# Performance work log

Hardware: AMD Instinct MI355X
Metric: run time of the kernel (lower is better)

The kernel has to match this reference:

```python
import jax, jax.numpy as jnp
import numpy as np

K = 24            # kNN neighbors per DynamicEdgeConv (includes self, dist 0)
N_PER_GRAPH = 128 # uniform nodes per graph
N_GRAPHS = 128
N_IN = 16
HID = 128
N_OUT = 6


def _knn_idx(xg, k):
    # xg: [G, N, D] -> indices of k nearest neighbors per node, [G, N, k]
    sq = jnp.sum(xg * xg, axis=-1)                       # [G, N]
    d2 = sq[:, :, None] + sq[:, None, :] - 2.0 * jnp.einsum('gnd,gmd->gnm', xg, xg)
    _, idx = jax.lax.top_k(-d2, k)                       # smallest distances
    return idx


def _dynamic_edge_conv(xg, w, b, k=K):
    # DynamicEdgeConv: recompute kNN on current features, edge MLP on
    # [x_i, x_j - x_i], max-aggregate over neighbors.
    idx = _knn_idx(xg, k)                                # [G, N, k]
    x_j = jax.vmap(lambda v, i: v[i])(xg, idx)           # [G, N, k, D]
    x_i = xg[:, :, None, :]                              # [G, N, 1, D]
    e = jnp.concatenate([jnp.broadcast_to(x_i, x_j.shape), x_j - x_i], axis=-1)
    h = jax.nn.elu(jnp.einsum('gnkf,fh->gnkh', e, w) + b)
    return jnp.max(h, axis=2)                            # [G, N, H]


def _linear(x, w, b):
    return x @ w + b


def setup_inputs() -> dict:
    key = jax.random.key(0)
    ks = jax.random.split(key, 16)

    def W(k, fi, fo):
        return (jax.random.normal(k, (fi, fo), dtype=jnp.float32) / np.sqrt(fi)).astype(jnp.float32)

    inp = {
        'x_pf': jax.random.normal(ks[0], (N_GRAPHS * N_PER_GRAPH, N_IN), dtype=jnp.float32),
        'enc_w1': W(ks[1], N_IN, HID),  'enc_b1': jnp.zeros((HID,), jnp.float32),
        'enc_w2': W(ks[2], HID, HID),   'enc_b2': jnp.zeros((HID,), jnp.float32),
        'conv1_w': W(ks[3], 2 * HID, HID), 'conv1_b': jnp.zeros((HID,), jnp.float32),
        'conv2_w': W(ks[4], 2 * HID, HID), 'conv2_b': jnp.zeros((HID,), jnp.float32),
        'conv3_w': W(ks[5], 2 * HID, HID), 'conv3_b': jnp.zeros((HID,), jnp.float32),
        'out_w1': W(ks[6], HID, 64), 'out_b1': jnp.zeros((64,), jnp.float32),
        'out_w2': W(ks[7], 64, 32),  'out_b2': jnp.zeros((32,), jnp.float32),
        'out_w3': W(ks[8], 32, 32),  'out_b3': jnp.zeros((32,), jnp.float32),
        'out_w4': W(ks[9], 32, N_OUT), 'out_b4': jnp.zeros((N_OUT,), jnp.float32),
        'batch_pf': jnp.repeat(jnp.arange(N_GRAPHS, dtype=jnp.int64 if jax.config.jax_enable_x64 else jnp.int32), N_PER_GRAPH),
    }
    return inp


def reference(x_pf, enc_w1, enc_b1, enc_w2, enc_b2,
              conv1_w, conv1_b, conv2_w, conv2_b, conv3_w, conv3_b,
              out_w1, out_b1, out_w2, out_b2, out_w3, out_b3, out_w4, out_b4,
              batch_pf):
    G = x_pf.shape[0] // N_PER_GRAPH
    # pf_encode: Linear -> ELU -> Linear -> ELU
    h = jax.nn.elu(_linear(x_pf, enc_w1, enc_b1))
    h = jax.nn.elu(_linear(h, enc_w2, enc_b2))
    hg = h.reshape(G, N_PER_GRAPH, HID)  # uniform graphs; batch_pf = repeat(arange(G))
    hg = _dynamic_edge_conv(hg, conv1_w, conv1_b)
    hg = _dynamic_edge_conv(hg, conv2_w, conv2_b)
    hg = _dynamic_edge_conv(hg, conv3_w, conv3_b)
    # global_add_pool over nodes of each graph
    pooled = jnp.sum(hg, axis=1)                          # [G, HID]
    o = jax.nn.elu(_linear(pooled, out_w1, out_b1))
    o = jax.nn.elu(_linear(o, out_w2, out_b2))
    o = jax.nn.elu(_linear(o, out_w3, out_b3))
    o = _linear(o, out_w4, out_b4)
    return (o, batch_pf)
```

## Files before the change

kernel.cpp:

```cpp
#include <hip/hip_runtime.h>
#include <hip/hip_fp16.h>
#include <hip/hip_bf16.h>
#include <cmath>

#define G_NUM 128
#define NPTS  128
#define FDIM  128
#define KNNK  24
#define NTOT  (G_NUM*NPTS)

typedef short s8v __attribute__((ext_vector_type(8)));
typedef float f32x4 __attribute__((ext_vector_type(4)));

__device__ __forceinline__ float eluf(float x){ return x > 0.0f ? x : expm1f(x); }

__device__ __forceinline__ unsigned short f2bf(float f) {
    unsigned int u = __float_as_uint(f);
    unsigned int r = (u + 0x7fffu + ((u >> 16) & 1u)) >> 16;
    return (unsigned short)r;
}
__device__ __forceinline__ float bf2f(unsigned short b) {
    return __uint_as_float(((unsigned int)b) << 16);
}

__global__ void prep_kernel(const float* __restrict__ w1, const float* __restrict__ w2,
                            const float* __restrict__ w3, const float* __restrict__ ew2,
                            const float* __restrict__ b1, const float* __restrict__ b2,
                            const float* __restrict__ b3,
                            unsigned short* __restrict__ wcatT,
                            unsigned short* __restrict__ enc2T,
                            float* __restrict__ bias,
                            const int* __restrict__ bpf,
                            float* __restrict__ out)
{
    int e = blockIdx.x * 256 + threadIdx.x;
    if (e < 16384) out[768 + e] = (float)bpf[e];
    if (e < 98304) {
        int l = e >> 15;
        int r = e & 32767;
        int k = r >> 8;
        int n = r & 255;
        const float* w = (l == 0) ? w1 : ((l == 1) ? w2 : w3);
        float v = (n < 128) ? (w[k * 128 + n] - w[(128 + k) * 128 + n])
                            : w[(128 + k) * 128 + (n - 128)];
        wcatT[l * 32768 + n * 128 + k] = f2bf(v);
    } else if (e < 114688) {
        int i = e - 98304;
        int k = i >> 7, n = i & 127;
        enc2T[n * 128 + k] = f2bf(ew2[k * 128 + n]);
    } else if (e < 115456) {
        int j = e - 114688;
        int l = j >> 8, c = j & 255;
        const float* b = (l == 0) ? b1 : ((l == 1) ? b2 : b3);
        bias[l * 256 + c] = (c < 128) ? b[c] : 0.0f;
    }
}

template<int DOELU>
__global__ __launch_bounds__(256) void gemmT(const float* __restrict__ A,
                                             const unsigned short* __restrict__ Bt,
                                             const float* __restrict__ bias,
                                             float* __restrict__ C0,
                                             float* __restrict__ C1)
{
    extern __shared__ char smc[];
    const int tid = threadIdx.x;
    const int m0 = blockIdx.x * 128;
    const unsigned short* Btg = Bt + (size_t)blockIdx.y * 16384;
    const float* bg = bias + blockIdx.y * 128;
    float* C = blockIdx.y ? C1 : C0;

    for (int e = tid; e < 4096; e += 256) {
        int m = e >> 5, q = e & 31;
        float4 v = *reinterpret_cast<const float4*>(&A[(size_t)(m0 + m) * 128 + 4 * q]);
        ushort4 p;
        p.x = f2bf(v.x); p.y = f2bf(v.y); p.z = f2bf(v.z); p.w = f2bf(v.w);
        int byte = (m * 256 + q * 8) ^ ((m & 15) << 4);
        *reinterpret_cast<ushort4*>(smc + byte) = p;
    }
    for (int e = tid; e < 2048; e += 256) {
        int n = e >> 4, q = e & 15;
        uint4 v = *reinterpret_cast<const uint4*>(Btg + n * 128 + q * 8);
        int byte = (n * 256 + q * 16) ^ ((n & 15) << 4);
        *reinterpret_cast<uint4*>(smc + 32768 + byte) = v;
    }
    __syncthreads();

    const int l = tid & 63, w = tid >> 6;
    const int wr = w >> 1, wc = w & 1;
    const int lr = l & 15, lg = l >> 4;

    f32x4 acc[4][4] = {};
    #pragma unroll
    for (int ks = 0; ks < 4; ++ks) {
        s8v a_f[4], b_f[4];
        #pragma unroll
        for (int mi = 0; mi < 4; ++mi) {
            int row = wr * 64 + mi * 16 + lr;
            int byte = (row * 256 + ks * 64 + lg * 16) ^ ((row & 15) << 4);
            a_f[mi] = *reinterpret_cast<const s8v*>(smc + byte);
        }
        #pragma unroll
        for (int ni = 0; ni < 4; ++ni) {
            int n = wc * 64 + ni * 16 + lr;
            int byte = (n * 256 + ks * 64 + lg * 16) ^ ((n & 15) << 4);
            b_f[ni] = *reinterpret_cast<const s8v*>(smc + 32768 + byte);
        }
        #pragma unroll
        for (int mi = 0; mi < 4; ++mi)
            #pragma unroll
            for (int ni = 0; ni < 4; ++ni)
                acc[mi][ni] = __builtin_amdgcn_mfma_f32_16x16x32_bf16(
                    a_f[mi], b_f[ni], acc[mi][ni], 0, 0, 0);
    }

    float bl[4];
    #pragma unroll
    for (int ni = 0; ni < 4; ++ni) bl[ni] = bg[wc * 64 + ni * 16 + lr];

    #pragma unroll
    for (int mi = 0; mi < 4; ++mi) {
        int rbase = m0 + wr * 64 + mi * 16 + lg * 4;
        #pragma unroll
        for (int ni = 0; ni < 4; ++ni) {
            int col = wc * 64 + ni * 16 + lr;
            #pragma unroll
            for (int q = 0; q < 4; ++q) {
                float v = acc[mi][ni][q] + bl[ni];
                if (DOELU) v = eluf(v);
                C[(size_t)(rbase + q) * 128 + col] = v;
            }
        }
    }
}

template<int KD, int TM, int DOELU>
__global__ __launch_bounds__(256) void gemm2(const float* __restrict__ A, int lda,
                                             const float* __restrict__ B, int ldb,
                                             const float* __restrict__ bias,
                                             float* __restrict__ C0)
{
    extern __shared__ float sm[];
    float* As = sm;
    float* Bs = sm + TM * (KD + 1);
    const int tid = threadIdx.x;
    const int m0 = blockIdx.x * TM;
    float* C = C0;
    const float* bg = bias;

    constexpr int NF4 = KD / 4;
    for (int e = tid; e < TM * NF4; e += 256) {
        int q = e % NF4, m = e / NF4;
        float4 v = *reinterpret_cast<const float4*>(&A[(size_t)(m0 + m) * lda + 4 * q]);
        float* dst = &As[m * (KD + 1) + 4 * q];
        dst[0] = v.x; dst[1] = v.y; dst[2] = v.z; dst[3] = v.w;
    }
    for (int e = tid; e < KD * 32; e += 256) {
        int q = e & 31, k = e >> 5;
        float4 v = *reinterpret_cast<const float4*>(&B[(size_t)k * ldb + 4 * q]);
        float* dst = &Bs[k * 129 + 4 * q];
        dst[0] = v.x; dst[1] = v.y; dst[2] = v.z; dst[3] = v.w;
    }
    __syncthreads();

    const int tml = tid & 15;
    const int tnh = tid >> 4;
    constexpr int NR = TM / 16;
    float acc[NR][8] = {};
    #pragma unroll 4
    for (int k = 0; k < KD; ++k) {
        float av[NR], bv[8];
        #pragma unroll
        for (int s = 0; s < NR; ++s) av[s] = As[(tml + 16 * s) * (KD + 1) + k];
        #pragma unroll
        for (int u = 0; u < 8; ++u) bv[u] = Bs[k * 129 + tnh + 16 * u];
        #pragma unroll
        for (int s = 0; s < NR; ++s)
            #pragma unroll
            for (int u = 0; u < 8; ++u) acc[s][u] += av[s] * bv[u];
    }
    __syncthreads();
    float* Ce = sm;
    #pragma unroll
    for (int s = 0; s < NR; ++s)
        #pragma unroll
        for (int u = 0; u < 8; ++u)
            Ce[(tml + 16 * s) * 132 + tnh + 16 * u] = acc[s][u];
    __syncthreads();
    for (int e = tid; e < TM * 32; e += 256) {
        int q = e & 31, m = e >> 5;
        float4 v = *reinterpret_cast<const float4*>(&Ce[m * 132 + 4 * q]);
        float4 b4 = *reinterpret_cast<const float4*>(&bg[4 * q]);
        v.x += b4.x; v.y += b4.y; v.z += b4.z; v.w += b4.w;
        if (DOELU) { v.x = eluf(v.x); v.y = eluf(v.y); v.z = eluf(v.z); v.w = eluf(v.w); }
        *reinterpret_cast<float4*>(&C[(size_t)(m0 + m) * 128 + 4 * q]) = v;
    }
}

#define XHI_OFF 0
#define XLO_OFF 32768
#define D_OFF   65536
#define SQ_OFF  99328
#define IDX_OFF 99840
#define CC_OFF  105984
#define EDGE_LDS 138752

__global__ __launch_bounds__(512) void edge_kernel(const float* __restrict__ hin,
                                                   const float* __restrict__ cc,
                                                   float* __restrict__ hio)
{
    extern __shared__ char smc[];
    float* D  = (float*)(smc + D_OFF);
    float* Sq = (float*)(smc + SQ_OFF);
    unsigned int* idxL = (unsigned int*)(smc + IDX_OFF);
    unsigned int* Cc   = (unsigned int*)(smc + CC_OFF);

    const int g = blockIdx.x >> 1, half = blockIdx.x & 1;
    const int r0 = half * 64;
    const int tid = threadIdx.x;
    const float* hg = hin + (size_t)g * NPTS * FDIM;
    const float* cg = cc  + (size_t)g * NPTS * FDIM;
    float* og = hio + (size_t)g * NPTS * FDIM;

    {
        const int m = tid >> 2;
        const int k0 = (tid & 3) * 32;
        float sq = 0.f;
        #pragma unroll
        for (int i = 0; i < 8; ++i) {
            float4 v = *reinterpret_cast<const float4*>(&hg[m * 128 + k0 + 4 * i]);
            ushort4 hi, lo;
            hi.x = f2bf(v.x); lo.x = f2bf(v.x - bf2f(hi.x));
            hi.y = f2bf(v.y); lo.y = f2bf(v.y - bf2f(hi.y));
            hi.z = f2bf(v.z); lo.z = f2bf(v.z - bf2f(hi.z));
            hi.w = f2bf(v.w); lo.w = f2bf(v.w - bf2f(hi.w));
            sq += v.x * v.x + v.y * v.y + v.z * v.z + v.w * v.w;
            int byte = (m * 256 + (k0 + 4 * i) * 2) ^ ((m & 15) << 4);
            *reinterpret_cast<ushort4*>(smc + XHI_OFF + byte) = hi;
            *reinterpret_cast<ushort4*>(smc + XLO_OFF + byte) = lo;
        }
        sq += __shfl_xor(sq, 1);
        sq += __shfl_xor(sq, 2);
        if ((tid & 3) == 0) Sq[m] = sq;
    }
    __syncthreads();

    if (tid < 256) {
        const int w = tid >> 6;
        const int l = tid & 63;
        const int lr = l & 15, lg = l >> 4;
        const int arow = r0 + w * 16 + lr;
        const int aswz = (arow & 15) << 4;

        f32x4 acc[8] = {};
        #pragma unroll
        for (int ks = 0; ks < 4; ++ks) {
            int abyte = (arow * 256 + ks * 64 + lg * 16) ^ aswz;
            s8v ahi = *reinterpret_cast<const s8v*>(smc + XHI_OFF + abyte);
            s8v alo = *reinterpret_cast<const s8v*>(smc + XLO_OFF + abyte);
            #pragma unroll
            for (int ni = 0; ni < 8; ++ni) {
                int brow = ni * 16 + lr;
                int bbyte = (brow * 256 + ks * 64 + lg * 16) ^ ((brow & 15) << 4);
                s8v bhi = *reinterpret_cast<const s8v*>(smc + XHI_OFF + bbyte);
                s8v blo = *reinterpret_cast<const s8v*>(smc + XLO_OFF + bbyte);
                acc[ni] = __builtin_amdgcn_mfma_f32_16x16x32_bf16(alo, bhi, acc[ni], 0, 0, 0);
                acc[ni] = __builtin_amdgcn_mfma_f32_16x16x32_bf16(ahi, blo, acc[ni], 0, 0, 0);
                acc[ni] = __builtin_amdgcn_mfma_f32_16x16x32_bf16(ahi, bhi, acc[ni], 0, 0, 0);
            }
        }
        float sqa[4];
        #pragma unroll
        for (int q = 0; q < 4; ++q) sqa[q] = Sq[r0 + w * 16 + lg * 4 + q];
        #pragma unroll
        for (int ni = 0; ni < 8; ++ni) {
            float sqc = Sq[ni * 16 + lr];
            #pragma unroll
            for (int q = 0; q < 4; ++q)
                D[(w * 16 + lg * 4 + q) * 132 + ni * 16 + lr] =
                    sqa[q] + sqc - 2.f * acc[ni][q];
        }
    } else {
        for (int e = tid - 256; e < 4096; e += 256) {
            int q = e & 31, j = e >> 5;
            float4 v = *reinterpret_cast<const float4*>(&cg[j * 128 + 4 * q]);
            unsigned int p0 = ((unsigned int)__half_as_ushort(__float2half(v.y)) << 16)
                            |  (unsigned int)__half_as_ushort(__float2half(v.x));
            unsigned int p1 = ((unsigned int)__half_as_ushort(__float2half(v.w)) << 16)
                            |  (unsigned int)__half_as_ushort(__float2half(v.z));
            Cc[j * 64 + 2 * q]     = p0;
            Cc[j * 64 + 2 * q + 1] = p1;
        }
    }
    __syncthreads();

    const int w8 = tid >> 6, l = tid & 63;

    for (int lr2 = w8 * 8; lr2 < w8 * 8 + 8; ++lr2) {
        float2 cur = *reinterpret_cast<const float2*>(&D[lr2 * 132 + 2 * l]);
        unsigned int ub0 = __float_as_uint(cur.x);
        unsigned int ub1 = __float_as_uint(cur.y);
        unsigned int u0 = (ub0 & 0x80000000u) ? ~ub0 : (ub0 | 0x80000000u);
        unsigned int u1 = (ub1 & 0x80000000u) ? ~ub1 : (ub1 | 0x80000000u);

        bool c0 = true, c1 = true, in0 = false, in1 = false;
        int need = KNNK;
        for (int b = 31; b >= 0; --b) {
            bool z0 = c0 && !((u0 >> b) & 1u);
            bool z1 = c1 && !((u1 >> b) & 1u);
            int cnt = __popcll(__ballot(z0)) + __popcll(__ballot(z1));
            if (cnt > need) { c0 = z0; c1 = z1; }
            else if (cnt == need) { in0 |= z0; in1 |= z1; need = 0; break; }
            else { in0 |= z0; in1 |= z1; need -= cnt;
                   c0 = c0 && !z0; c1 = c1 && !z1; }
        }
        if (need > 0) {
            unsigned long long m0 = __ballot(c0), m1 = __ballot(c1);
            unsigned long long below = (1ull << l) - 1ull;
            int rk0 = __popcll(m0 & below) + __popcll(m1 & below);
            int rk1 = rk0 + (int)((m0 >> l) & 1ull);
            in0 = in0 || (c0 && rk0 < need);
            in1 = in1 || (c1 && rk1 < need);
        }
        unsigned long long f0 = __ballot(in0), f1 = __ballot(in1);
        int cnt0 = __popcll(f0);
        unsigned long long below = (1ull << l) - 1ull;
        if (in0) idxL[lr2 * KNNK + __popcll(f0 & below)] = 2 * l;
        if (in1) idxL[lr2 * KNNK + cnt0 + __popcll(f1 & below)] = 2 * l + 1;
    }

    {
        const int hh = l >> 5, j = l & 31;
        #pragma unroll
        for (int u = 0; u < 4; ++u) {
            const int r = w8 * 8 + 2 * u + hh;
            const unsigned int* il = &idxL[r * KNNK];
            float mc0 = -3.0e38f, mc1 = -3.0e38f, mc2 = -3.0e38f, mc3 = -3.0e38f;
            #pragma unroll
            for (int t = 0; t < KNNK; t += 4) {
                unsigned int p0 = il[t], p1 = il[t + 1], p2 = il[t + 2], p3 = il[t + 3];
                uint2 a = *reinterpret_cast<const uint2*>(&Cc[p0 * 64 + 2 * j]);
                uint2 b = *reinterpret_cast<const uint2*>(&Cc[p1 * 64 + 2 * j]);
                uint2 c = *reinterpret_cast<const uint2*>(&Cc[p2 * 64 + 2 * j]);
                uint2 d = *reinterpret_cast<const uint2*>(&Cc[p3 * 64 + 2 * j]);
                mc0 = fmaxf(fmaxf(mc0,
                        __half2float(__ushort_as_half((unsigned short)(a.x & 0xffffu)))),
                        fmaxf(__half2float(__ushort_as_half((unsigned short)(b.x & 0xffffu))),
                              fmaxf(__half2float(__ushort_as_half((unsigned short)(c.x & 0xffffu))),
                                    __half2float(__ushort_as_half((unsigned short)(d.x & 0xffffu))))));
                mc1 = fmaxf(fmaxf(mc1,
                        __half2float(__ushort_as_half((unsigned short)(a.x >> 16)))),
                        fmaxf(__half2float(__ushort_as_half((unsigned short)(b.x >> 16))),
                              fmaxf(__half2float(__ushort_as_half((unsigned short)(c.x >> 16))),
                                    __half2float(__ushort_as_half((unsigned short)(d.x >> 16))))));
                mc2 = fmaxf(fmaxf(mc2,
                        __half2float(__ushort_as_half((unsigned short)(a.y & 0xffffu)))),
                        fmaxf(__half2float(__ushort_as_half((unsigned short)(b.y & 0xffffu))),
                              fmaxf(__half2float(__ushort_as_half((unsigned short)(c.y & 0xffffu))),
                                    __half2float(__ushort_as_half((unsigned short)(d.y & 0xffffu))))));
                mc3 = fmaxf(fmaxf(mc3,
                        __half2float(__ushort_as_half((unsigned short)(a.y >> 16)))),
                        fmaxf(__half2float(__ushort_as_half((unsigned short)(b.y >> 16))),
                              fmaxf(__half2float(__ushort_as_half((unsigned short)(c.y >> 16))),
                                    __half2float(__ushort_as_half((unsigned short)(d.y >> 16))))));
            }
            float4 av = *reinterpret_cast<const float4*>(&og[(r0 + r) * 128 + 4 * j]);
            float4 o;
            o.x = eluf(av.x + mc0);
            o.y = eluf(av.y + mc1);
            o.z = eluf(av.z + mc2);
            o.w = eluf(av.w + mc3);
            *reinterpret_cast<float4*>(&og[(r0 + r) * 128 + 4 * j]) = o;
        }
    }
}

__global__ __launch_bounds__(512) void head_kernel(const float* __restrict__ h,
        const float* __restrict__ w1, const float* __restrict__ b1,
        const float* __restrict__ w2, const float* __restrict__ b2,
        const float* __restrict__ w3, const float* __restrict__ b3,
        const float* __restrict__ w4, const float* __restrict__ b4,
        float* __restrict__ out)
{
    __shared__ float ps[4][128];
    __shared__ float pooled[128], s1[64], s2[32], s3[32];
    const int g = blockIdx.x, t = threadIdx.x;
    const float* hg = h + (size_t)g * NPTS * FDIM;
    const int f = t & 127, hp = t >> 7;
    float s = 0.0f;
    for (int p = 0; p < 32; ++p) s += hg[(hp * 32 + p) * 128 + f];
    ps[hp][f] = s;
    __syncthreads();
    if (t < 128) pooled[t] = ps[0][t] + ps[1][t] + ps[2][t] + ps[3][t];
    __syncthreads();
    if (t < 64) {
        float a = b1[t];
        #pragma unroll 8
        for (int k = 0; k < 128; ++k) a += pooled[k] * w1[k * 64 + t];
        s1[t] = eluf(a);
    }
    __syncthreads();
    if (t < 32) {
        float a = b2[t];
        #pragma unroll 8
        for (int k = 0; k < 64; ++k) a += s1[k] * w2[k * 32 + t];
        s2[t] = eluf(a);
    }
    __syncthreads();
    if (t < 32) {
        float a = b3[t];
        #pragma unroll 8
        for (int k = 0; k < 32; ++k) a += s2[k] * w3[k * 32 + t];
        s3[t] = eluf(a);
    }
    __syncthreads();
    if (t < 6) {
        float a = b4[t];
        #pragma unroll 8
        for (int k = 0; k < 32; ++k) a += s3[k] * w4[k * 6 + t];
        out[g * 6 + t] = a;
    }
}

extern "C" void kernel_launch(void* const* d_in, const int* in_sizes, int n_in,
                              void* d_out, int out_size, void* d_ws, size_t ws_size,
                              hipStream_t stream)
{
    const float* x_pf   = (const float*)d_in[0];
    const float* enc_w1 = (const float*)d_in[1];
    const float* enc_b1 = (const float*)d_in[2];
    const float* enc_w2 = (const float*)d_in[3];
    const float* enc_b2 = (const float*)d_in[4];
    const float* c1w = (const float*)d_in[5];
    const float* c1b = (const float*)d_in[6];
    const float* c2w = (const float*)d_in[7];
    const float* c2b = (const float*)d_in[8];
    const float* c3w = (const float*)d_in[9];
    const float* c3b = (const float*)d_in[10];
    const float* o_w1 = (const float*)d_in[11];
    const float* o_b1 = (const float*)d_in[12];
    const float* o_w2 = (const float*)d_in[13];
    const float* o_b2 = (const float*)d_in[14];
    const float* o_w3 = (const float*)d_in[15];
    const float* o_b3 = (const float*)d_in[16];
    const float* o_w4 = (const float*)d_in[17];
    const float* o_b4 = (const float*)d_in[18];
    const int*   bpf  = (const int*)d_in[19];
    float* out = (float*)d_out;

    float* ws   = (float*)d_ws;
    float* h_a  = ws;
    float* h_b  = h_a + (size_t)NTOT * FDIM;
    float* ac_c = h_b + (size_t)NTOT * FDIM;
    unsigned short* wcatT = (unsigned short*)(ac_c + (size_t)NTOT * FDIM);
    unsigned short* enc2T = wcatT + 3 * 32768;
    float* biasF = (float*)(enc2T + 16384);

    prep_kernel<<<451, 256, 0, stream>>>(c1w, c2w, c3w, enc_w2,
                                         c1b, c2b, c3b, wcatT, enc2T, biasF,
                                         bpf, out);

    gemm2<16, 64, 1><<<dim3(NTOT / 64, 1), 256, 8448 * 4, stream>>>(
        x_pf, 16, enc_w1, 128, enc_b1, ac_c);
    gemmT<1><<<dim3(NTOT / 128, 1), 256, 65536, stream>>>(
        ac_c, enc2T, enc_b2, h_a, nullptr);

    float* hc = h_a;
    float* hn = h_b;
    for (int l = 0; l < 3; ++l) {
        gemmT<0><<<dim3(NTOT / 128, 2), 256, 65536, stream>>>(
            hc, wcatT + (size_t)l * 32768, biasF + l * 256, hn, ac_c);
        edge_kernel<<<2 * G_NUM, 512, EDGE_LDS, stream>>>(hc, ac_c, hn);
        float* t = hc; hc = hn; hn = t;
    }

    head_kernel<<<G_NUM, 512, 0, stream>>>(hc, o_w1, o_b1, o_w2, o_b2, o_w3, o_b3,
                                           o_w4, o_b4, out);
}
```

Baseline: 298.8 us.

## Fuse per-layer edge-conv GEMMs into the kNN/aggregation kernel

Removes the separate gemmT launch that computed x_i-part and x_j-part projections to global memory. The edge kernel now computes both projections in-block with MFMA from the bf16 node features already in LDS, reading weights straight from global. The neighbor projections go to fp16 in LDS and the self term to fp32 in LDS. This cuts global round-trips and one launch per layer, at the cost of redundant neighbor-projection work across the two half-graph blocks and uncached weight loads. LDS row padding is also changed to reduce bank conflicts.

```diff
diff --git a/kernel.cpp b/kernel.cpp
--- a/kernel.cpp
+++ b/kernel.cpp
@@ -60,15 +60,12 @@
 __global__ __launch_bounds__(256) void gemmT(const float* __restrict__ A,
                                              const unsigned short* __restrict__ Bt,
                                              const float* __restrict__ bias,
-                                             float* __restrict__ C0,
-                                             float* __restrict__ C1)
+                                             float* __restrict__ C0)
 {
     extern __shared__ char smc[];
     const int tid = threadIdx.x;
     const int m0 = blockIdx.x * 128;
-    const unsigned short* Btg = Bt + (size_t)blockIdx.y * 16384;
-    const float* bg = bias + blockIdx.y * 128;
-    float* C = blockIdx.y ? C1 : C0;
+    float* C = C0;
 
     for (int e = tid; e < 4096; e += 256) {
         int m = e >> 5, q = e & 31;
@@ -80,7 +77,7 @@
     }
     for (int e = tid; e < 2048; e += 256) {
         int n = e >> 4, q = e & 15;
-        uint4 v = *reinterpret_cast<const uint4*>(Btg + n * 128 + q * 8);
+        uint4 v = *reinterpret_cast<const uint4*>(Bt + n * 128 + q * 8);
         int byte = (n * 256 + q * 16) ^ ((n & 15) << 4);
         *reinterpret_cast<uint4*>(smc + 32768 + byte) = v;
     }
@@ -116,7 +113,7 @@
 
     float bl[4];
     #pragma unroll
-    for (int ni = 0; ni < 4; ++ni) bl[ni] = bg[wc * 64 + ni * 16 + lr];
+    for (int ni = 0; ni < 4; ++ni) bl[ni] = bias[wc * 64 + ni * 16 + lr];
 
     #pragma unroll
     for (int mi = 0; mi < 4; ++mi) {
@@ -200,27 +197,28 @@
 #define XHI_OFF 0
 #define XLO_OFF 32768
 #define D_OFF   65536
-#define SQ_OFF  99328
-#define IDX_OFF 99840
-#define CC_OFF  105984
-#define EDGE_LDS 138752
-
-__global__ __launch_bounds__(512) void edge_kernel(const float* __restrict__ hin,
-                                                   const float* __restrict__ cc,
-                                                   float* __restrict__ hio)
+#define CC_OFF  98816
+#define IDX_OFF 132608
+#define SQ_OFF  138752
+#define CONV_LDS 139264
+
+__global__ __launch_bounds__(512) void conv_fused(const float* __restrict__ hin,
+                                                  const unsigned short* __restrict__ wT,
+                                                  const float* __restrict__ bias,
+                                                  float* __restrict__ hout)
 {
     extern __shared__ char smc[];
     float* D  = (float*)(smc + D_OFF);
     float* Sq = (float*)(smc + SQ_OFF);
     unsigned int* idxL = (unsigned int*)(smc + IDX_OFF);
     unsigned int* Cc   = (unsigned int*)(smc + CC_OFF);
+    float* Al = (float*)(smc + XLO_OFF);
 
     const int g = blockIdx.x >> 1, half = blockIdx.x & 1;
     const int r0 = half * 64;
     const int tid = threadIdx.x;
     const float* hg = hin + (size_t)g * NPTS * FDIM;
-    const float* cg = cc  + (size_t)g * NPTS * FDIM;
-    float* og = hio + (size_t)g * NPTS * FDIM;
+    float* og = hout + (size_t)g * NPTS * FDIM;
 
     {
         const int m = tid >> 2;
@@ -245,13 +243,12 @@
     }
     __syncthreads();
 
-    if (tid < 256) {
-        const int w = tid >> 6;
-        const int l = tid & 63;
-        const int lr = l & 15, lg = l >> 4;
+    const int l = tid & 63, w = tid >> 6;
+    const int lr = l & 15, lg = l >> 4;
+
+    if (w < 4) {
         const int arow = r0 + w * 16 + lr;
         const int aswz = (arow & 15) << 4;
-
         f32x4 acc[8] = {};
         #pragma unroll
         for (int ks = 0; ks < 4; ++ks) {
@@ -277,27 +274,79 @@
             float sqc = Sq[ni * 16 + lr];
             #pragma unroll
             for (int q = 0; q < 4; ++q)
-                D[(w * 16 + lg * 4 + q) * 132 + ni * 16 + lr] =
+                D[(w * 16 + lg * 4 + q) * 130 + ni * 16 + lr] =
                     sqa[q] + sqc - 2.f * acc[ni][q];
         }
     } else {
-        for (int e = tid - 256; e < 4096; e += 256) {
-            int q = e & 31, j = e >> 5;
-            float4 v = *reinterpret_cast<const float4*>(&cg[j * 128 + 4 * q]);
-            unsigned int p0 = ((unsigned int)__half_as_ushort(__float2half(v.y)) << 16)
-                            |  (unsigned int)__half_as_ushort(__float2half(v.x));
-            unsigned int p1 = ((unsigned int)__half_as_ushort(__float2half(v.w)) << 16)
-                            |  (unsigned int)__half_as_ushort(__float2half(v.z));
-            Cc[j * 64 + 2 * q]     = p0;
-            Cc[j * 64 + 2 * q + 1] = p1;
-        }
-    }
-    __syncthreads();
-
-    const int w8 = tid >> 6, l = tid & 63;
-
-    for (int lr2 = w8 * 8; lr2 < w8 * 8 + 8; ++lr2) {
-        float2 cur = *reinterpret_cast<const float2*>(&D[lr2 * 132 + 2 * l]);
+        const int w4 = w - 4;
+        f32x4 acc[2][8] = {};
+        #pragma unroll
+        for (int ks = 0; ks < 4; ++ks) {
+            s8v a_f[2];
+            #pragma unroll
+            for (int m2 = 0; m2 < 2; ++m2) {
+                int row = (2 * w4 + m2) * 16 + lr;
+                int byte = (row * 256 + ks * 64 + lg * 16) ^ ((row & 15) << 4);
+                a_f[m2] = *reinterpret_cast<const s8v*>(smc + XHI_OFF + byte);
+            }
+            #pragma unroll
+            for (int ni = 0; ni < 8; ++ni) {
+                int n = 128 + ni * 16 + lr;
+                s8v b = *reinterpret_cast<const s8v*>(wT + n * 128 + ks * 32 + lg * 8);
+                #pragma unroll
+                for (int m2 = 0; m2 < 2; ++m2)
+                    acc[m2][ni] = __builtin_amdgcn_mfma_f32_16x16x32_bf16(
+                        a_f[m2], b, acc[m2][ni], 0, 0, 0);
+            }
+        }
+        #pragma unroll
+        for (int m2 = 0; m2 < 2; ++m2)
+            #pragma unroll
+            for (int ni = 0; ni < 8; ++ni)
+                #pragma unroll
+                for (int q = 0; q < 4; ++q) {
+                    float v = acc[m2][ni][q];
+                    float p = __shfl_xor(v, 1);
+                    if (!(lr & 1)) {
+                        unsigned int u =
+                            ((unsigned int)__half_as_ushort(__float2half(p)) << 16)
+                          |  (unsigned int)__half_as_ushort(__float2half(v));
+                        int j = (2 * w4 + m2) * 16 + lg * 4 + q;
+                        Cc[j * 66 + ni * 8 + (lr >> 1)] = u;
+                    }
+                }
+    }
+    __syncthreads();
+
+    {
+        const int mt = w >> 1;
+        const int nb = (w & 1) * 4;
+        f32x4 acc[4] = {};
+        const int arow = r0 + mt * 16 + lr;
+        const int aswz = (arow & 15) << 4;
+        #pragma unroll
+        for (int ks = 0; ks < 4; ++ks) {
+            int abyte = (arow * 256 + ks * 64 + lg * 16) ^ aswz;
+            s8v a_f = *reinterpret_cast<const s8v*>(smc + XHI_OFF + abyte);
+            #pragma unroll
+            for (int ni = 0; ni < 4; ++ni) {
+                int n = (nb + ni) * 16 + lr;
+                s8v b = *reinterpret_cast<const s8v*>(wT + n * 128 + ks * 32 + lg * 8);
+                acc[ni] = __builtin_amdgcn_mfma_f32_16x16x32_bf16(a_f, b, acc[ni], 0, 0, 0);
+            }
+        }
+        #pragma unroll
+        for (int ni = 0; ni < 4; ++ni) {
+            int h = (nb + ni) * 16 + lr;
+            float bl = bias[h];
+            #pragma unroll
+            for (int q = 0; q < 4; ++q)
+                Al[(mt * 16 + lg * 4 + q) * 128 + h] = acc[ni][q] + bl;
+        }
+    }
+
+    for (int lr2 = w * 8; lr2 < w * 8 + 8; ++lr2) {
+        float2 cur = *reinterpret_cast<const float2*>(&D[lr2 * 130 + 2 * l]);
         unsigned int ub0 = __float_as_uint(cur.x);
         unsigned int ub1 = __float_as_uint(cur.y);
         unsigned int u0 = (ub0 & 0x80000000u) ? ~ub0 : (ub0 | 0x80000000u);
@@ -328,21 +377,22 @@
         if (in0) idxL[lr2 * KNNK + __popcll(f0 & below)] = 2 * l;
         if (in1) idxL[lr2 * KNNK + cnt0 + __popcll(f1 & below)] = 2 * l + 1;
     }
+    __syncthreads();
 
     {
-        const int hh = l >> 5, j = l & 31;
+        const int hh = l >> 5, jl = l & 31;
         #pragma unroll
         for (int u = 0; u < 4; ++u) {
-            const int r = w8 * 8 + 2 * u + hh;
+            const int r = w * 8 + 2 * u + hh;
             const unsigned int* il = &idxL[r * KNNK];
             float mc0 = -3.0e38f, mc1 = -3.0e38f, mc2 = -3.0e38f, mc3 = -3.0e38f;
             #pragma unroll
             for (int t = 0; t < KNNK; t += 4) {
                 unsigned int p0 = il[t], p1 = il[t + 1], p2 = il[t + 2], p3 = il[t + 3];
-                uint2 a = *reinterpret_cast<const uint2*>(&Cc[p0 * 64 + 2 * j]);
-                uint2 b = *reinterpret_cast<const uint2*>(&Cc[p1 * 64 + 2 * j]);
-                uint2 c = *reinterpret_cast<const uint2*>(&Cc[p2 * 64 + 2 * j]);
-                uint2 d = *reinterpret_cast<const uint2*>(&Cc[p3 * 64 + 2 * j]);
+                uint2 a = *reinterpret_cast<const uint2*>(&Cc[p0 * 66 + 2 * jl]);
+                uint2 b = *reinterpret_cast<const uint2*>(&Cc[p1 * 66 + 2 * jl]);
+                uint2 c = *reinterpret_cast<const uint2*>(&Cc[p2 * 66 + 2 * jl]);
+                uint2 d = *reinterpret_cast<const uint2*>(&Cc[p3 * 66 + 2 * jl]);
                 mc0 = fmaxf(fmaxf(mc0,
                         __half2float(__ushort_as_half((unsigned short)(a.x & 0xffffu)))),
                         fmaxf(__half2float(__ushort_as_half((unsigned short)(b.x & 0xffffu))),
@@ -364,13 +414,13 @@
                               fmaxf(__half2float(__ushort_as_half((unsigned short)(c.y >> 16))),
                                     __half2float(__ushort_as_half((unsigned short)(d.y >> 16))))));
             }
-            float4 av = *reinterpret_cast<const float4*>(&og[(r0 + r) * 128 + 4 * j]);
+            float4 av = *reinterpret_cast<const float4*>(&Al[r * 128 + 4 * jl]);
             float4 o;
             o.x = eluf(av.x + mc0);
             o.y = eluf(av.y + mc1);
             o.z = eluf(av.z + mc2);
             o.w = eluf(av.w + mc3);
-            *reinterpret_cast<float4*>(&og[(r0 + r) * 128 + 4 * j]) = o;
+            *reinterpret_cast<float4*>(&og[(r0 + r) * 128 + 4 * jl]) = o;
         }
     }
 }
@@ -463,14 +513,13 @@
     gemm2<16, 64, 1><<<dim3(NTOT / 64, 1), 256, 8448 * 4, stream>>>(
         x_pf, 16, enc_w1, 128, enc_b1, ac_c);
     gemmT<1><<<dim3(NTOT / 128, 1), 256, 65536, stream>>>(
-        ac_c, enc2T, enc_b2, h_a, nullptr);
+        ac_c, enc2T, enc_b2, h_a);
 
     float* hc = h_a;
     float* hn = h_b;
     for (int l = 0; l < 3; ++l) {
-        gemmT<0><<<dim3(NTOT / 128, 2), 256, 65536, stream>>>(
-            hc, wcatT + (size_t)l * 32768, biasF + l * 256, hn, ac_c);
-        edge_kernel<<<2 * G_NUM, 512, EDGE_LDS, stream>>>(hc, ac_c, hn);
+        conv_fused<<<2 * G_NUM, 512, CONV_LDS, stream>>>(
+            hc, wcatT + (size_t)l * 32768, biasF + l * 256, hn);
         float* t = hc; hc = hn; hn = t;
     }
 
```

Result: faster. 292.5 us (-2.1%).
